# Kernel optimization log

Measured on AMD Instinct MI355X. Metric: run time of the kernel, lower is better.

The kernel has to match this reference:

```python
import jax, jax.numpy as jnp
import numpy as np


def setup_inputs() -> dict:
    key = jax.random.key(0)
    ks = jax.random.split(key, 5)
    B, S, E2, D = 64, 1024, 1024, 512  # E2 = 2*enc_hid_dim
    hidden = jax.random.normal(ks[0], (B, D), dtype=jnp.float32)
    encoder_outputs = jax.random.normal(ks[1], (B, S, E2), dtype=jnp.float32)
    mask = jnp.ones((B, S), dtype=jnp.int32)
    attn_W = jax.random.normal(ks[2], (E2 + D, D), dtype=jnp.float32) * 0.02
    attn_b = jax.random.normal(ks[3], (D,), dtype=jnp.float32) * 0.02
    v_W = jax.random.normal(ks[4], (D,), dtype=jnp.float32) * 0.02
    return {"hidden": hidden, "encoder_outputs": encoder_outputs, "mask": mask,
            "attn_W": attn_W, "attn_b": attn_b, "v_W": v_W}


def reference(hidden, encoder_outputs, mask, attn_W, attn_b, v_W):
    # cat((hidden_repeated, enc_out)) @ attn_W  ==  hidden @ W_h + enc_out @ W_e
    D = hidden.shape[-1]
    W_h = attn_W[-D:]          # [D, D]   (decoder-hidden part of concat)
    W_e = attn_W[:-D]          # [2E, D]  (encoder-output part)
    # Note: torch concat order is (hidden, encoder_outputs), so split accordingly.
    W_hid = attn_W[: D] if False else attn_W[:D]
    # concat order: hidden first -> rows [0:D] are hidden's, rows [D:] are encoder's
    W_h = attn_W[:D]           # [D, D]
    W_e = attn_W[D:]           # [2E, D]
    h_proj = hidden @ W_h                                   # [B, D]
    e_proj = jnp.einsum('bse,ed->bsd', encoder_outputs, W_e)  # [B, S, D]
    energy = jnp.tanh(e_proj + h_proj[:, None, :] + attn_b)   # [B, S, D]
    scores = jnp.einsum('bsd,d->bs', energy, v_W)             # [B, S]
    neg_inf = jnp.finfo(scores.dtype).min
    scores = jnp.where(mask == 0, neg_inf, scores)
    attn_weights = jax.nn.softmax(scores, axis=1)             # [B, S]
    context = jnp.einsum('bs,bse->be', attn_weights, encoder_outputs)  # [B, 2E]
    return context, attn_weights
```

## Files before the change

### kernel.cpp

```cpp
#include <hip/hip_runtime.h>
#include <hip/hip_bf16.h>


typedef __attribute__((ext_vector_type(4))) float f32x4;
typedef __attribute__((ext_vector_type(8))) short short8;
typedef __attribute__((ext_vector_type(8))) __bf16 bf16x8;

__device__ __forceinline__ void gload_lds16(const void* g, void* l) {
  __builtin_amdgcn_global_load_lds(
      (const __attribute__((address_space(1))) unsigned int*)g,
      (__attribute__((address_space(3))) unsigned int*)l,
      16, 0, 0);
}

__device__ __forceinline__ unsigned short f2bf_rne(float f) {
  union { float f; unsigned int u; } v; v.f = f;
  unsigned int r = v.u + 0x7FFFu + ((v.u >> 16) & 1u);
  return (unsigned short)(r >> 16);
}

__device__ __forceinline__ float fast_tanh(float x) {
  float e = __expf(2.0f * x);
  return 1.0f - 2.0f * __builtin_amdgcn_rcpf(e + 1.0f);
}

__global__ void hproj_kernel(const float* __restrict__ hidden,
                             const float* __restrict__ attn_W,
                             float* __restrict__ hb ) {
  int b = blockIdx.x >> 2, kc = blockIdx.x & 3;
  int tid = threadIdx.x;
  __shared__ float hrow[128];
  if (tid < 128) hrow[tid] = hidden[b * 512 + kc * 128 + tid];
  __syncthreads();
  const float* Wp = attn_W + (size_t)(kc * 128) * 512;
  float a0 = 0.f, a1 = 0.f;
#pragma unroll 4
  for (int k = 0; k < 128; ++k) {
    float h = hrow[k];
    a0 = fmaf(h, Wp[(size_t)k * 512 + tid], a0);
    a1 = fmaf(h, Wp[(size_t)k * 512 + tid + 256], a1);
  }
  atomicAdd(&hb[b * 512 + tid], a0);
  atomicAdd(&hb[b * 512 + tid + 256], a1);
}

__global__ void wet_kernel(const float* __restrict__ attn_W,
                           unsigned short* __restrict__ weT) {
  __shared__ float tile[64][65];
  int bx = blockIdx.x;
  int kt = bx & 15;
  int nt = bx >> 4;
  int tid = threadIdx.x;
  int j = tid & 63, i = tid >> 6;
  const float* src = attn_W + (size_t)(512 + kt * 64) * 512 + nt * 64;
#pragma unroll
  for (int p = 0; p < 16; ++p) {
    int r = p * 4 + i;
    tile[r][j] = src[(size_t)r * 512 + j];
  }
  __syncthreads();
  unsigned short* dst = weT + (size_t)(nt * 64) * 1024 + kt * 64;
#pragma unroll
  for (int p = 0; p < 16; ++p) {
    int c = p * 4 + i;
    dst[(size_t)c * 1024 + j] = f2bf_rne(tile[j][c]);
  }
}

__global__ __launch_bounds__(256) void fused_score_gemm(
    const float* __restrict__ enc,
    const unsigned short* __restrict__ weT,
    const float* __restrict__ hb,
    const float* __restrict__ attn_b,
    const float* __restrict__ vW,
    float* __restrict__ scores)
{
  __shared__ float At[128 * 64];
  __shared__ unsigned short Bt[128 * 64];

  int bx = blockIdx.x;
  int wg = ((bx & 7) << 8) | (bx >> 3);
  int m0 = (wg >> 2) << 7;
  int n0 = (wg & 3) << 7;

  int tid = threadIdx.x;
  int w = tid >> 6, l = tid & 63;
  int g = l >> 4, l15 = l & 15;
  int wm = (w >> 1) << 6, wn = (w & 1) << 6;

  int aSrc[8];
#pragma unroll
  for (int i = 0; i < 8; ++i) {
    int c = ((i * 4 + w) << 6) | l;
    int row = c >> 4, s16 = c & 15;
    aSrc[i] = row * 1024 + ((s16 ^ (row & 7)) << 2);
  }
  int bSrc[4];
#pragma unroll
  for (int i = 0; i < 4; ++i) {
    int c = ((i * 4 + w) << 6) | l;
    int row = c >> 3, s16 = c & 7;
    bSrc[i] = row * 1024 + ((s16 ^ (row & 7)) << 3);
  }

  const float* Ab = enc + (size_t)m0 * 1024;
  const unsigned short* Bb = weT + (size_t)n0 * 1024;

  f32x4 zero = {0.f, 0.f, 0.f, 0.f};
  f32x4 acc[4][4];
#pragma unroll
  for (int i = 0; i < 4; ++i)
#pragma unroll
    for (int j = 0; j < 4; ++j) acc[i][j] = zero;

  int aRd[4][2][2], bRd[4][2];
#pragma unroll
  for (int mt = 0; mt < 4; ++mt) {
    int row = wm + mt * 16 + l15;
#pragma unroll
    for (int kk = 0; kk < 2; ++kk) {
      int s = kk * 8 + g * 2;
      aRd[mt][kk][0] = row * 256 + ((s ^ (row & 7)) << 4);
      aRd[mt][kk][1] = row * 256 + (((s + 1) ^ (row & 7)) << 4);
    }
  }
#pragma unroll
  for (int nt = 0; nt < 4; ++nt) {
    int row = wn + nt * 16 + l15;
#pragma unroll
    for (int kk = 0; kk < 2; ++kk) {
      int s = kk * 4 + g;
      bRd[nt][kk] = row * 128 + ((s ^ (row & 7)) << 4);
    }
  }

  const char* Atc = (const char*)At;
  const char* Btc = (const char*)Bt;

  for (int kt = 0; kt < 16; ++kt) {
    int k0 = kt << 6;
#pragma unroll
    for (int i = 0; i < 8; ++i)
      gload_lds16(Ab + aSrc[i] + k0, (char*)At + ((i * 4 + w) << 10));
#pragma unroll
    for (int i = 0; i < 4; ++i)
      gload_lds16(Bb + bSrc[i] + k0, (char*)Bt + ((i * 4 + w) << 10));
    __syncthreads();

#pragma unroll
    for (int kk = 0; kk < 2; ++kk) {
      short8 af[4], bfr[4];
#pragma unroll
      for (int mt = 0; mt < 4; ++mt) {
        f32x4 lo = *(const f32x4*)(Atc + aRd[mt][kk][0]);
        f32x4 hi = *(const f32x4*)(Atc + aRd[mt][kk][1]);
        bf16x8 a;
        a[0] = (__bf16)lo[0]; a[1] = (__bf16)lo[1];
        a[2] = (__bf16)lo[2]; a[3] = (__bf16)lo[3];
        a[4] = (__bf16)hi[0]; a[5] = (__bf16)hi[1];
        a[6] = (__bf16)hi[2]; a[7] = (__bf16)hi[3];
        af[mt] = __builtin_bit_cast(short8, a);
      }
#pragma unroll
      for (int nt = 0; nt < 4; ++nt)
        bfr[nt] = *(const short8*)(Btc + bRd[nt][kk]);
#pragma unroll
      for (int mt = 0; mt < 4; ++mt)
#pragma unroll
        for (int nt = 0; nt < 4; ++nt)
          acc[mt][nt] = __builtin_amdgcn_mfma_f32_16x16x32_bf16(
              af[mt], bfr[nt], acc[mt][nt], 0, 0, 0);
    }
    __syncthreads();
  }

  int b = m0 >> 10;
  float hbv[4], vwv[4];
#pragma unroll
  for (int nt = 0; nt < 4; ++nt) {
    int d = n0 + wn + nt * 16 + l15;
    hbv[nt] = hb[(b << 9) + d] + attn_b[d];
    vwv[nt] = vW[d];
  }
#pragma unroll
  for (int mt = 0; mt < 4; ++mt) {
#pragma unroll
    for (int j = 0; j < 4; ++j) {
      float p = 0.f;
#pragma unroll
      for (int nt = 0; nt < 4; ++nt)
        p = fmaf(fast_tanh(acc[mt][nt][j] + hbv[nt]), vwv[nt], p);
      p += __shfl_xor(p, 1);
      p += __shfl_xor(p, 2);
      p += __shfl_xor(p, 4);
      p += __shfl_xor(p, 8);
      if (l15 == 0)
        atomicAdd(&scores[m0 + wm + mt * 16 + (g << 2) + j], p);
    }
  }
}

__global__ void softmax_kernel(const float* __restrict__ scores,
                               const int* __restrict__ mask,
                               float* __restrict__ attn_out) {
  int b = blockIdx.x, tid = threadIdx.x;
  __shared__ float red[256];
  const float NEG = -3.402823466e38f;
  float v[4];
  float mx = NEG;
#pragma unroll
  for (int i = 0; i < 4; ++i) {
    int s = (i << 8) + tid;
    float sc = scores[(b << 10) + s];
    v[i] = (mask[(b << 10) + s] == 0) ? NEG : sc;
    mx = fmaxf(mx, v[i]);
  }
  red[tid] = mx; __syncthreads();
  for (int off = 128; off > 0; off >>= 1) {
    if (tid < off) red[tid] = fmaxf(red[tid], red[tid + off]);
    __syncthreads();
  }
  mx = red[0]; __syncthreads();
  float sum = 0.f;
#pragma unroll
  for (int i = 0; i < 4; ++i) { v[i] = __expf(v[i] - mx); sum += v[i]; }
  red[tid] = sum; __syncthreads();
  for (int off = 128; off > 0; off >>= 1) {
    if (tid < off) red[tid] += red[tid + off];
    __syncthreads();
  }
  float inv = 1.f / red[0];
#pragma unroll
  for (int i = 0; i < 4; ++i)
    attn_out[(b << 10) + (i << 8) + tid] = v[i] * inv;
}

__global__ void context_kernel(const float* __restrict__ wts,
                               const float* __restrict__ enc,
                               float* __restrict__ ctx ) {
  int bx = blockIdx.x;
  int b = bx >> 4, ech = (bx >> 2) & 3, sch = bx & 3;
  int e = (ech << 8) + threadIdx.x;
  const float* encp = enc + (size_t)((b << 10) + (sch << 8)) * 1024 + e;
  const float* wp = wts + (b << 10) + (sch << 8);
  float a0 = 0.f, a1 = 0.f, a2 = 0.f, a3 = 0.f;
  for (int s = 0; s < 256; s += 4) {
    a0 = fmaf(wp[s + 0], encp[(size_t)(s + 0) << 10], a0);
    a1 = fmaf(wp[s + 1], encp[(size_t)(s + 1) << 10], a1);
    a2 = fmaf(wp[s + 2], encp[(size_t)(s + 2) << 10], a2);
    a3 = fmaf(wp[s + 3], encp[(size_t)(s + 3) << 10], a3);
  }
  atomicAdd(&ctx[(b << 10) + e], a0 + a1 + a2 + a3);
}

extern "C" void kernel_launch(void* const* d_in, const int* in_sizes, int n_in,
                              void* d_out, int out_size, void* d_ws, size_t ws_size,
                              hipStream_t stream) {
  const float* hidden = (const float*)d_in[0];
  const float* enc    = (const float*)d_in[1];
  const int*   mask   = (const int*)d_in[2];
  const float* attn_W = (const float*)d_in[3];
  const float* attn_b = (const float*)d_in[4];
  const float* vW     = (const float*)d_in[5];
  float* out = (float*)d_out;

  float* scores = (float*)d_ws;
  float* hb     = scores + 65536;
  unsigned short* weT = (unsigned short*)(hb + 32768);

  hipMemsetAsync(d_ws, 0, (65536 + 32768) * sizeof(float), stream);
  hipMemsetAsync(d_out, 0, 65536 * sizeof(float), stream);

  hproj_kernel<<<256, 256, 0, stream>>>(hidden, attn_W, hb);
  wet_kernel<<<128, 256, 0, stream>>>(attn_W, weT);
  fused_score_gemm<<<2048, 256, 0, stream>>>(enc, weT, hb, attn_b, vW, scores);
  softmax_kernel<<<64, 256, 0, stream>>>(scores, mask, out + 65536);
  context_kernel<<<1024, 256, 0, stream>>>(out + 65536, enc, out);
}
```

Measured before the change: 509.5 us.

## Stage A through registers as bf16 with prefetch; vectorize context kernel

```diff
diff --git a/kernel.cpp b/kernel.cpp
--- a/kernel.cpp
+++ b/kernel.cpp
@@ -67,7 +67,7 @@
   }
 }
 
-__global__ __launch_bounds__(256) void fused_score_gemm(
+__global__ __launch_bounds__(256, 4) void fused_score_gemm(
     const float* __restrict__ enc,
     const unsigned short* __restrict__ weT,
     const float* __restrict__ hb,
@@ -75,7 +75,7 @@
     const float* __restrict__ vW,
     float* __restrict__ scores)
 {
-  __shared__ float At[128 * 64];
+  __shared__ unsigned short At[128 * 64];
   __shared__ unsigned short Bt[128 * 64];
 
   int bx = blockIdx.x;
@@ -88,20 +88,15 @@
   int g = l >> 4, l15 = l & 15;
   int wm = (w >> 1) << 6, wn = (w & 1) << 6;
 
-  int aSrc[8];
-#pragma unroll
-  for (int i = 0; i < 8; ++i) {
-    int c = ((i * 4 + w) << 6) | l;
-    int row = c >> 4, s16 = c & 15;
-    aSrc[i] = row * 1024 + ((s16 ^ (row & 7)) << 2);
-  }
-  int bSrc[4];
-#pragma unroll
-  for (int i = 0; i < 4; ++i) {
-    int c = ((i * 4 + w) << 6) | l;
-    int row = c >> 3, s16 = c & 7;
-    bSrc[i] = row * 1024 + ((s16 ^ (row & 7)) << 3);
-  }
+  int arow = tid >> 3;
+  int aps = tid & 7;
+  int asg = aps ^ (arow & 7);
+  int aoff0 = arow * 1024 + asg * 8;
+
+  int brow = ((w << 6) | l) >> 3;
+  int bps = l & 7;
+  int bsg = bps ^ ((l >> 3) & 7);
+  int boff0 = brow * 1024 + bsg * 8;
 
   const float* Ab = enc + (size_t)m0 * 1024;
   const unsigned short* Bb = weT + (size_t)n0 * 1024;
@@ -113,65 +108,67 @@
 #pragma unroll
     for (int j = 0; j < 4; ++j) acc[i][j] = zero;
 
-  int aRd[4][2][2], bRd[4][2];
+  int aRd[4], bRd[4];
 #pragma unroll
   for (int mt = 0; mt < 4; ++mt) {
     int row = wm + mt * 16 + l15;
-#pragma unroll
-    for (int kk = 0; kk < 2; ++kk) {
-      int s = kk * 8 + g * 2;
-      aRd[mt][kk][0] = row * 256 + ((s ^ (row & 7)) << 4);
-      aRd[mt][kk][1] = row * 256 + (((s + 1) ^ (row & 7)) << 4);
-    }
+    aRd[mt] = row * 128 + ((g ^ (row & 7)) << 4);
   }
 #pragma unroll
   for (int nt = 0; nt < 4; ++nt) {
     int row = wn + nt * 16 + l15;
-#pragma unroll
-    for (int kk = 0; kk < 2; ++kk) {
-      int s = kk * 4 + g;
-      bRd[nt][kk] = row * 128 + ((s ^ (row & 7)) << 4);
-    }
+    bRd[nt] = row * 128 + ((g ^ (row & 7)) << 4);
   }
 
   const char* Atc = (const char*)At;
   const char* Btc = (const char*)Bt;
 
+  f32x4 rA[8];
+#pragma unroll
+  for (int i = 0; i < 4; ++i) {
+    rA[2 * i]     = *(const f32x4*)(Ab + aoff0 + i * 32768);
+    rA[2 * i + 1] = *(const f32x4*)(Ab + aoff0 + i * 32768 + 4);
+  }
+
   for (int kt = 0; kt < 16; ++kt) {
-    int k0 = kt << 6;
-#pragma unroll
-    for (int i = 0; i < 8; ++i)
-      gload_lds16(Ab + aSrc[i] + k0, (char*)At + ((i * 4 + w) << 10));
+    int k0n = (kt + (kt < 15)) << 6;
+    __syncthreads();
+#pragma unroll
+    for (int i = 0; i < 4; ++i) {
+      bf16x8 v;
+      v[0] = (__bf16)rA[2 * i][0]; v[1] = (__bf16)rA[2 * i][1];
+      v[2] = (__bf16)rA[2 * i][2]; v[3] = (__bf16)rA[2 * i][3];
+      v[4] = (__bf16)rA[2 * i + 1][0]; v[5] = (__bf16)rA[2 * i + 1][1];
+      v[6] = (__bf16)rA[2 * i + 1][2]; v[7] = (__bf16)rA[2 * i + 1][3];
+      *(short8*)((char*)At + (i << 12) + (tid << 4)) = __builtin_bit_cast(short8, v);
+    }
 #pragma unroll
     for (int i = 0; i < 4; ++i)
-      gload_lds16(Bb + bSrc[i] + k0, (char*)Bt + ((i * 4 + w) << 10));
-    __syncthreads();
-
+      gload_lds16(Bb + boff0 + i * 32768 + (kt << 6),
+                  (char*)Bt + ((i * 4 + w) << 10));
+    __syncthreads();
+#pragma unroll
+    for (int i = 0; i < 4; ++i) {
+      rA[2 * i]     = *(const f32x4*)(Ab + aoff0 + i * 32768 + k0n);
+      rA[2 * i + 1] = *(const f32x4*)(Ab + aoff0 + i * 32768 + k0n + 4);
+    }
 #pragma unroll
     for (int kk = 0; kk < 2; ++kk) {
-      short8 af[4], bfr[4];
-#pragma unroll
-      for (int mt = 0; mt < 4; ++mt) {
-        f32x4 lo = *(const f32x4*)(Atc + aRd[mt][kk][0]);
-        f32x4 hi = *(const f32x4*)(Atc + aRd[mt][kk][1]);
-        bf16x8 a;
-        a[0] = (__bf16)lo[0]; a[1] = (__bf16)lo[1];
-        a[2] = (__bf16)lo[2]; a[3] = (__bf16)lo[3];
-        a[4] = (__bf16)hi[0]; a[5] = (__bf16)hi[1];
-        a[6] = (__bf16)hi[2]; a[7] = (__bf16)hi[3];
-        af[mt] = __builtin_bit_cast(short8, a);
-      }
+      int kx = kk << 6;
+      short8 af[4], bfm[4];
+#pragma unroll
+      for (int mt = 0; mt < 4; ++mt)
+        af[mt] = *(const short8*)(Atc + (aRd[mt] ^ kx));
 #pragma unroll
       for (int nt = 0; nt < 4; ++nt)
-        bfr[nt] = *(const short8*)(Btc + bRd[nt][kk]);
+        bfm[nt] = *(const short8*)(Btc + (bRd[nt] ^ kx));
 #pragma unroll
       for (int mt = 0; mt < 4; ++mt)
 #pragma unroll
         for (int nt = 0; nt < 4; ++nt)
           acc[mt][nt] = __builtin_amdgcn_mfma_f32_16x16x32_bf16(
-              af[mt], bfr[nt], acc[mt][nt], 0, 0, 0);
-    }
-    __syncthreads();
+              af[mt], bfm[nt], acc[mt][nt], 0, 0, 0);
+    }
   }
 
   int b = m0 >> 10;
@@ -239,18 +236,29 @@
                                const float* __restrict__ enc,
                                float* __restrict__ ctx ) {
   int bx = blockIdx.x;
-  int b = bx >> 4, ech = (bx >> 2) & 3, sch = bx & 3;
-  int e = (ech << 8) + threadIdx.x;
-  const float* encp = enc + (size_t)((b << 10) + (sch << 8)) * 1024 + e;
-  const float* wp = wts + (b << 10) + (sch << 8);
-  float a0 = 0.f, a1 = 0.f, a2 = 0.f, a3 = 0.f;
-  for (int s = 0; s < 256; s += 4) {
-    a0 = fmaf(wp[s + 0], encp[(size_t)(s + 0) << 10], a0);
-    a1 = fmaf(wp[s + 1], encp[(size_t)(s + 1) << 10], a1);
-    a2 = fmaf(wp[s + 2], encp[(size_t)(s + 2) << 10], a2);
-    a3 = fmaf(wp[s + 3], encp[(size_t)(s + 3) << 10], a3);
-  }
-  atomicAdd(&ctx[(b << 10) + e], a0 + a1 + a2 + a3);
+  int b = bx >> 4, sch = bx & 15;
+  int tid = threadIdx.x;
+  const float* encp = enc + ((size_t)(b << 10) + (sch << 6)) * 1024 + (tid << 2);
+  const float* wp = wts + (b << 10) + (sch << 6);
+  f32x4 a0 = {0.f, 0.f, 0.f, 0.f}, a1 = a0, a2 = a0, a3 = a0;
+  for (int s = 0; s < 64; s += 4) {
+    float w0 = wp[s], w1 = wp[s + 1], w2 = wp[s + 2], w3 = wp[s + 3];
+    f32x4 v0 = *(const f32x4*)(encp + ((size_t)(s + 0) << 10));
+    f32x4 v1 = *(const f32x4*)(encp + ((size_t)(s + 1) << 10));
+    f32x4 v2 = *(const f32x4*)(encp + ((size_t)(s + 2) << 10));
+    f32x4 v3 = *(const f32x4*)(encp + ((size_t)(s + 3) << 10));
+#pragma unroll
+    for (int j = 0; j < 4; ++j) {
+      a0[j] = fmaf(w0, v0[j], a0[j]);
+      a1[j] = fmaf(w1, v1[j], a1[j]);
+      a2[j] = fmaf(w2, v2[j], a2[j]);
+      a3[j] = fmaf(w3, v3[j], a3[j]);
+    }
+  }
+  float* dst = ctx + (b << 10) + (tid << 2);
+#pragma unroll
+  for (int j = 0; j < 4; ++j)
+    atomicAdd(&dst[j], a0[j] + a1[j] + a2[j] + a3[j]);
 }
 
 extern "C" void kernel_launch(void* const* d_in, const int* in_sizes, int n_in,
```

Result: faster. 485.3 us (-4.7%).
